# Optimization experiments

Hardware: AMD Instinct MI355X
Metric: run time of the kernel (lower is better)

Reference implementation:

```python
import jax, jax.numpy as jnp
import numpy as np

B = 4; IN_CH = 256; HEAD_CH = 64; NUM_CLS = 3; H = 128; W = 128
NH = 4; KEY = 16; VAL = 16; OUT_CH = 2
VX = 0.1 * 8; VY = 0.1 * 8  # voxel_size[:2] * out_size_factor
DW = 1.6; DL = 3.9; STRIDE = 1
C_CTR = (HEAD_CH + 2 + NUM_CLS) * 9      # 621
C_COR = (HEAD_CH + 2 + NUM_CLS * 4) * 8  # 624
C_FG = (HEAD_CH + 2 + NUM_CLS) * 9       # 621


def _sampler_points():
    offs = np.arange(-STRIDE, STRIDE + 1, STRIDE, dtype=np.float32)
    oy, ox = np.meshgrid(offs, offs, indexing='ij')
    ctr = np.stack([ox, oy], 0).reshape(2, 9)  # pixel offsets
    cx = np.array([-DW/2, -DW/2, DW/2, DW/2, DL/2, -DL/2, DL/2, -DL/2], np.float32) / VX
    cy = np.array([DL/2, -DL/2, DL/2, -DL/2, -DW/2, -DW/2, DW/2, DW/2], np.float32) / VY
    # faithful to torch: stack(dim=1) -> [8,2] then .view(2,8) (row-major reinterpret)
    cor = np.stack([cx, cy], 1).reshape(2, 8)
    r = max(DW, DL)
    fx = np.array([-r/3, -r/3, -r/3, 0, 0, 0, r/3, r/3, r/3], np.float32) / VX
    fy = np.array([-r/3, 0, r/3, -r/3, 0, r/3, -r/3, 0, r/3], np.float32) / VY
    fg = np.stack([fx, fy], 1).reshape(2, 9)
    return jnp.asarray(ctr), jnp.asarray(cor), jnp.asarray(fg)


def _raw_grid():
    gx = jnp.arange(W, dtype=jnp.float32) + 0.5
    gy = jnp.arange(H, dtype=jnp.float32) + 0.5
    return jnp.stack([jnp.broadcast_to(gx[None, :], (H, W)),
                      jnp.broadcast_to(gy[:, None], (H, W))], 0)  # [2,H,W]


def _conv3x3(x, w, b):
    y = jax.lax.conv_general_dilated(x, w, (1, 1), 'SAME',
                                     dimension_numbers=('NCHW', 'OIHW', 'NCHW'))
    return y + b[None, :, None, None]


def _cbr3(x, w, b, s, t):  # conv3x3 + inference-mode BN (folded scale/shift) + relu
    return jax.nn.relu(_conv3x3(x, w, b) * s[None, :, None, None] + t[None, :, None, None])


def _cbr1(x, w, b, s, t):  # per-head 1x1 conv + BN + relu, w: [NH,O,C], x: [B,C,H,W]
    y = jnp.einsum('noc,bchw->nbohw', w, x) + b[:, None, :, None, None]
    return jax.nn.relu(y * s[:, None, :, None, None] + t[:, None, :, None, None])


def _sample(feats, grids):
    # feats [B,C,H,W]; grids [2,n,H,W] pixel coords. Matches F.grid_sample
    # (bilinear, zeros padding, align_corners=False): sample at pixel coord g-0.5.
    n = grids.shape[1]
    geo = jnp.stack([grids[0] / W, grids[1] / H], 0)  # recover_coords, [2,n,H,W]
    gx, gy = grids[0] - 0.5, grids[1] - 0.5
    x0f = jnp.floor(gx); y0f = jnp.floor(gy)
    dx, dy = gx - x0f, gy - y0f
    x0 = x0f.astype(jnp.int32); y0 = y0f.astype(jnp.int32)
    flat = feats.reshape(B, -1, H * W)

    def gather(xc, yc, wgt):
        valid = ((xc >= 0) & (xc < W) & (yc >= 0) & (yc < H)).astype(feats.dtype) * wgt
        idx = jnp.clip(yc, 0, H - 1) * W + jnp.clip(xc, 0, W - 1)
        v = jnp.take(flat, idx.reshape(-1), axis=2).reshape(B, -1, n, H, W)
        return v * valid[None, None]

    s = (gather(x0, y0, (1 - dx) * (1 - dy)) + gather(x0 + 1, y0, dx * (1 - dy))
         + gather(x0, y0 + 1, (1 - dx) * dy) + gather(x0 + 1, y0 + 1, dx * dy))
    geo_b = jnp.broadcast_to(geo[None], (B,) + geo.shape)
    out = jnp.concatenate([s, geo_b], axis=1)  # [B,C+2,n,H,W]
    return out.reshape(B, -1, H, W)           # channel index = c*n + p, as torch .view


def _forward(base_feats, cc_w, cc_b, cc_s, cc_t, ch_w, ch_b,
             oc_w, oc_b, oc_s, oc_t, oh_w, oh_b,
             fc_w, fc_b, fc_s, fc_t, fh_w, fh_b,
             q_w, q_b, q_s, q_t,
             ck_w, ck_b, ck_s, ck_t, cv_w, cv_b, cv_s, cv_t,
             kk_w, kk_b, kk_s, kk_t, kv_w, kv_b, kv_s, kv_t,
             fk_w, fk_b, fk_s, fk_t, fv_w, fv_b, fv_s, fv_t,
             p1_w, p1_b, p1_s, p1_t, p2_w, p2_b):
    center_feat = _cbr3(base_feats, cc_w, cc_b, cc_s, cc_t)
    center_map = _conv3x3(center_feat, ch_w, ch_b)
    corner_feat = _cbr3(base_feats, oc_w, oc_b, oc_s, oc_t)
    corner_map = _conv3x3(corner_feat, oh_w, oh_b)
    fg_feat = _cbr3(base_feats, fc_w, fc_b, fc_s, fc_t)
    fg_map = _conv3x3(fg_feat, fh_w, fh_b)

    ctr_pts, cor_pts, fg_pts = _sampler_points()
    raw = _raw_grid()
    g_ctr = raw[:, None] + ctr_pts[:, :, None, None]  # [2,9,H,W]
    g_cor = raw[:, None] + cor_pts[:, :, None, None]  # [2,8,H,W]
    g_fg = raw[:, None] + fg_pts[:, :, None, None]    # [2,9,H,W]

    cs = _sample(jnp.concatenate([center_feat, center_map], 1), g_ctr)  # [B,621,H,W]
    os_ = _sample(jnp.concatenate([corner_feat, corner_map], 1), g_cor)  # [B,624,H,W]
    fs = _sample(jnp.concatenate([fg_feat, fg_map], 1), g_fg)            # [B,621,H,W]

    q = _cbr1(base_feats, q_w, q_b, q_s, q_t)  # [NH,B,KEY,H,W]
    ck = _cbr1(cs, ck_w, ck_b, ck_s, ck_t); cv = _cbr1(cs, cv_w, cv_b, cv_s, cv_t)
    ok = _cbr1(os_, kk_w, kk_b, kk_s, kk_t); ov = _cbr1(os_, kv_w, kv_b, kv_s, kv_t)
    fk = _cbr1(fs, fk_w, fk_b, fk_s, fk_t); fv = _cbr1(fs, fv_w, fv_b, fv_s, fv_t)

    logits = jnp.stack([(q * ck).sum(2), (q * ok).sum(2), (q * fk).sum(2)], axis=2)  # [NH,B,3,H,W]
    attw = jax.nn.softmax(logits, axis=2)
    vals = jnp.stack([cv, ov, fv], axis=2)          # [NH,B,3,VAL,H,W]
    att = (attw[:, :, :, None] * vals).sum(2)       # [NH,B,VAL,H,W]

    # predict: 1x1 conv over cat([base_feats, att]) + BN + relu, then 1x1 to out_ch
    h1 = (jnp.einsum('noc,bchw->nbohw', p1_w[:, :, :IN_CH], base_feats)
          + jnp.einsum('nov,nbvhw->nbohw', p1_w[:, :, IN_CH:], att)
          + p1_b[:, None, :, None, None])
    h1 = jax.nn.relu(h1 * p1_s[:, None, :, None, None] + p1_t[:, None, :, None, None])
    pred = jnp.einsum('npo,nbohw->nbphw', p2_w, h1) + p2_b[:, None, :, None, None]
    heads = jnp.moveaxis(pred, 0, 1).reshape(B, NH * OUT_CH, H, W)
    return jnp.concatenate([center_map, corner_map, fg_map, heads], axis=1)  # [B,26,H,W]


def setup_inputs() -> dict:
    ks = iter(jax.random.split(jax.random.key(0), 80))

    def rn(shape, s=0.05):
        return jax.random.normal(next(ks), shape, jnp.float32) * s

    d = {"base_feats": jax.random.normal(next(ks), (B, IN_CH, H, W), jnp.float32)}
    for conv, head, hc in (("cc", "ch", NUM_CLS), ("oc", "oh", NUM_CLS * 4), ("fc", "fh", NUM_CLS)):
        d[conv + "_w"] = rn((HEAD_CH, IN_CH, 3, 3)); d[conv + "_b"] = rn((HEAD_CH,))
        d[conv + "_s"] = 1.0 + rn((HEAD_CH,)); d[conv + "_t"] = rn((HEAD_CH,))
        d[head + "_w"] = rn((hc, HEAD_CH, 3, 3)); d[head + "_b"] = jnp.full((hc,), -2.19, jnp.float32)
    d["q_w"] = rn((NH, KEY, IN_CH)); d["q_b"] = rn((NH, KEY))
    d["q_s"] = 1.0 + rn((NH, KEY)); d["q_t"] = rn((NH, KEY))
    for name, cin, cout in (("ck", C_CTR, KEY), ("cv", C_CTR, VAL), ("kk", C_COR, KEY),
                            ("kv", C_COR, VAL), ("fk", C_FG, KEY), ("fv", C_FG, VAL)):
        d[name + "_w"] = rn((NH, cout, cin)); d[name + "_b"] = rn((NH, cout))
        d[name + "_s"] = 1.0 + rn((NH, cout)); d[name + "_t"] = rn((NH, cout))
    d["p1_w"] = rn((NH, HEAD_CH, IN_CH + VAL)); d["p1_b"] = rn((NH, HEAD_CH))
    d["p1_s"] = 1.0 + rn((NH, HEAD_CH)); d["p1_t"] = rn((NH, HEAD_CH))
    d["p2_w"] = rn((NH, OUT_CH, HEAD_CH)); d["p2_b"] = jnp.full((NH, OUT_CH), -2.19, jnp.float32)
    return d


def reference(base_feats, cc_w, cc_b, cc_s, cc_t, ch_w, ch_b,
              oc_w, oc_b, oc_s, oc_t, oh_w, oh_b,
              fc_w, fc_b, fc_s, fc_t, fh_w, fh_b,
              q_w, q_b, q_s, q_t,
              ck_w, ck_b, ck_s, ck_t, cv_w, cv_b, cv_s, cv_t,
              kk_w, kk_b, kk_s, kk_t, kv_w, kv_b, kv_s, kv_t,
              fk_w, fk_b, fk_s, fk_t, fv_w, fv_b, fv_s, fv_t,
              p1_w, p1_b, p1_s, p1_t, p2_w, p2_b):
    return _forward(base_feats, cc_w, cc_b, cc_s, cc_t, ch_w, ch_b,
                    oc_w, oc_b, oc_s, oc_t, oh_w, oh_b,
                    fc_w, fc_b, fc_s, fc_t, fh_w, fh_b,
                    q_w, q_b, q_s, q_t,
                    ck_w, ck_b, ck_s, ck_t, cv_w, cv_b, cv_s, cv_t,
                    kk_w, kk_b, kk_s, kk_t, kv_w, kv_b, kv_s, kv_t,
                    fk_w, fk_b, fk_s, fk_t, fv_w, fv_b, fv_s, fv_t,
                    p1_w, p1_b, p1_s, p1_t, p2_w, p2_b)
```

## Files before the change

### kernel.cpp

```cpp
#include <hip/hip_runtime.h>
#include <hip/hip_bf16.h>
#include <math.h>


#define HW 16384
#define WIMG 128

typedef unsigned short ushortT;
typedef __attribute__((ext_vector_type(8))) short short8;
typedef __attribute__((ext_vector_type(4))) float floatx4;
typedef __attribute__((ext_vector_type(4))) unsigned uintx4;

constexpr size_t OFF_KV    = 16777216;
constexpr size_t OFF_A16   = 29360128;
constexpr size_t OFF_B16   = 38012928;
constexpr size_t OFF_CWT   = 46057216;
constexpr size_t OFF_CB    = OFF_CWT + 221184;
constexpr size_t OFF_HWT   = OFF_CB + 192;
constexpr size_t OFF_QWT   = OFF_HWT + 13824;
constexpr size_t OFF_QB    = OFF_QWT + 8192;
constexpr size_t OFF_KVW   = OFF_QB + 64;
constexpr size_t OFF_GEO   = OFF_KVW + 266240;
constexpr size_t OFF_P1WT  = OFF_GEO + 1152;
constexpr size_t OFF_P1B   = OFF_P1WT + 40960;

struct P53 { const float* p[53]; };

__device__ inline ushortT f2bf(float f) {
    unsigned u = __float_as_uint(f);
    unsigned r = (u + 0x7FFFu + ((u >> 16) & 1u)) >> 16;
    return (ushortT)r;
}
__device__ inline unsigned packbf(float a, float b) {
    return (unsigned)f2bf(a) | ((unsigned)f2bf(b) << 16);
}
__device__ inline float bf2f(ushortT u) {
    return __uint_as_float((unsigned)u << 16);
}

typedef __attribute__((address_space(3))) ushortT lds_us;
typedef __attribute__((address_space(1))) const ushortT glb_us;
__device__ inline void gload_lds16(const ushortT* g, ushortT* ldsbase) {
    __builtin_amdgcn_global_load_lds((glb_us*)g, (lds_us*)ldsbase, 16, 0, 0);
}

__device__ const float c_ox[3][9] = {
    {-1.f, 0.f, 1.f, -1.f, 0.f, 1.f, -1.f, 0.f, 1.f},
    {-1.f, 2.4375f, -1.f, -2.4375f, 1.f, 2.4375f, 1.f, -2.4375f, 0.f},
    {-1.625f, -1.625f, -1.625f, 0.f, -1.625f, 1.625f, 0.f, -1.625f, 0.f}};
__device__ const float c_oy[3][9] = {
    {-1.f, -1.f, -1.f, 0.f, 0.f, 0.f, 1.f, 1.f, 1.f},
    {2.4375f, -1.f, -2.4375f, -1.f, 2.4375f, 1.f, -2.4375f, 1.f, 0.f},
    {0.f, 0.f, 1.625f, 1.625f, -1.625f, 1.625f, 0.f, 1.625f, 1.625f}};

__device__ const int tapX_cor[16] = {-1,-1, 2, 3,-1,-1,-3,-2, 1, 1, 2, 3, 1, 1,-3,-2};
__device__ const int tapY_cor[16] = { 2, 3,-1,-1,-3,-2,-1,-1, 2, 3, 1, 1,-3,-2, 1, 1};
__device__ const int tapR_cor[16] = { 4, 5, 2, 2, 0, 1, 2, 2, 4, 5, 3, 3, 0, 1, 3, 3};

__device__ inline float cornw(float off, int X) {
    float f = floorf(off);
    float d = off - f;
    int fi = (int)f;
    return (X == fi) ? (1.f - d) : (X == fi + 1) ? d : 0.f;
}

__global__ __launch_bounds__(256) void setup_kernel(P53 ptrs, float* __restrict__ ws,
                                                    const float* __restrict__ base,
                                                    ushortT* __restrict__ a16,
                                                    ushortT* __restrict__ b16) {
    int i = blockIdx.x * 256 + threadIdx.x;
    const float* const* p = ptrs.p;
    if (i < 1102464) {
        if (i < 442368) {
            int tap = i / 49152, r = i % 49152;
            int g = r / 1536, r2 = r % 1536;
            int M = r2 >> 3, j = r2 & 7;
            int br = M >> 6, oc = M & 63, ic = g * 8 + j;
            float v = p[1 + 6 * br][(oc * 256 + ic) * 9 + tap] * p[3 + 6 * br][oc];
            ((ushortT*)(ws + OFF_CWT))[i] = f2bf(v);
            return;
        }
        i -= 442368;
        if (i < 192) {
            int br = i >> 6, oc = i & 63;
            ws[OFF_CB + i] = p[2 + 6 * br][oc] * p[3 + 6 * br][oc] + p[4 + 6 * br][oc];
            return;
        }
        i -= 192;
        if (i < 27648) {
            int j = i & 7, m = (i >> 3) & 15, u = (i >> 7) % 72, br = i / 9216;
            int cnt = (br == 1) ? 12 : 3;
            int t = u >> 3, g = u & 7, ic = g * 8 + j;
            const float* hw = (br == 0) ? p[5] : (br == 1) ? p[11] : p[17];
            float v = (m < cnt) ? hw[(m * 64 + ic) * 9 + t] : 0.f;
            ((ushortT*)(ws + OFF_HWT))[i] = f2bf(v);
            return;
        }
        i -= 27648;
        if (i < 16384) {
            int j = i & 7, m = (i >> 3) & 63, sg = i >> 9;
            int k = (sg >> 2) * 32 + (sg & 3) * 8 + j;
            ((ushortT*)(ws + OFF_QWT))[i] = f2bf(p[19][m * 256 + k] * p[21][m]);
            return;
        }
        i -= 16384;
        if (i < 64) { ws[OFF_QB + i] = p[20][i] * p[21][i] + p[22][i]; return; }
        i -= 64;
        if (i < 532480) {
            int br, NQ, NTAP, n, C, i2;
            if (i < 110592)      { br = 0; NQ = 3; NTAP = 9;  n = 9; C = 67; i2 = i; }
            else if (i < 274432) { br = 1; NQ = 4; NTAP = 16; n = 8; C = 76; i2 = i - 110592; }
            else                 { br = 2; NQ = 7; NTAP = 25; n = 9; C = 67; i2 = i - 274432; }
            int gsz = NQ * 4096;
            int g = i2 / gsz, r = i2 % gsz;
            int q = r >> 12, r2 = r & 4095;
            int sub = r2 >> 10, m = (r2 >> 3) & 127, j = r2 & 7;
            int t = q * 4 + sub, c = g * 8 + j;
            float v = 0.f;
            if (t < NTAP && c < C) {
                int X, Y;
                if (br == 0)      { X = t % 3 - 1; Y = t / 3 - 1; }
                else if (br == 1) { X = tapX_cor[t]; Y = tapY_cor[t]; }
                else              { X = t % 5 - 2; Y = t / 5 - 2; }
                const float* wsrc = (m < 64) ? p[23 + 8 * br] : p[27 + 8 * br];
                int mo = (m < 64) ? m : m - 64;
                float sc = (m < 64) ? p[25 + 8 * br][mo] : p[29 + 8 * br][mo];
                int Cn = (C + 2) * n;
                float s = 0.f;
                for (int pp = 0; pp < n; ++pp) {
                    float ww = cornw(c_ox[br][pp], X) * cornw(c_oy[br][pp], Y);
                    if (ww != 0.f) s += ww * wsrc[mo * Cn + c * n + pp];
                }
                v = s * sc;
            }
            ((ushortT*)(ws + OFF_KVW))[i] = f2bf(v);
            return;
        }
        i -= 532480;
        if (i < 1152) {
            int br = i / 384, rem = i % 384, which = rem >> 7, m = rem & 127;
            int n = (br == 1) ? 8 : 9, C = (br == 1) ? 76 : 67, Cn = (C + 2) * n;
            const float* wsrc = (m < 64) ? p[23 + 8 * br] : p[27 + 8 * br];
            int mo = (m < 64) ? m : m - 64;
            float sc = (m < 64) ? p[25 + 8 * br][mo] : p[29 + 8 * br][mo];
            float bb = (m < 64) ? p[24 + 8 * br][mo] : p[28 + 8 * br][mo];
            float tt = (m < 64) ? p[26 + 8 * br][mo] : p[30 + 8 * br][mo];
            float v = 0.f;
            if (which == 0) {
                for (int pp = 0; pp < n; ++pp) v += wsrc[mo * Cn + C * n + pp];
                v *= sc;
            } else if (which == 1) {
                for (int pp = 0; pp < n; ++pp) v += wsrc[mo * Cn + (C + 1) * n + pp];
                v *= sc;
            } else {
                for (int pp = 0; pp < n; ++pp)
                    v += wsrc[mo * Cn + C * n + pp] * c_ox[br][pp]
                       + wsrc[mo * Cn + (C + 1) * n + pp] * c_oy[br][pp];
                v = v * sc * 0.0078125f + bb * sc + tt;
            }
            ws[OFF_GEO + br * 384 + which * 128 + m] = v;
            return;
        }
        i -= 1152;
        if (i < 81920) {
            int j = i & 7, M = (i >> 3) & 255, sg = i >> 11;
            int k = (sg >> 2) * 32 + (sg & 3) * 8 + j;
            int nh = M >> 6, oc = M & 63;
            float sc = p[49][nh * 64 + oc];
            float v;
            if (k < 256) v = p[47][(nh * 64 + oc) * 272 + k] * sc;
            else {
                int k2 = k - 256, nh2 = k2 >> 4, va = k2 & 15;
                v = (nh2 == nh) ? p[47][(nh * 64 + oc) * 272 + 256 + va] * sc : 0.f;
            }
            ((ushortT*)(ws + OFF_P1WT))[i] = f2bf(v);
            return;
        }
        i -= 81920;
        if (i < 256) { ws[OFF_P1B + i] = p[48][i] * p[49][i] + p[50][i]; }
        return;
    }
    int idx = i - 1102464;
    if (idx < 4 * 32 * 130 * 130) {
        int col = idx % 130, t = idx / 130;
        int row = t % 130; t /= 130;
        int icg = t & 31, b = t >> 5;
        int h = row - 1, w = col - 1;
        unsigned wds[4] = {0u, 0u, 0u, 0u};
        if ((unsigned)h < 128u && (unsigned)w < 128u) {
            const float* s = base + (size_t)(b * 256 + icg * 8) * HW + h * WIMG + w;
            #pragma unroll
            for (int jp = 0; jp < 4; ++jp)
                wds[jp] = packbf(s[(size_t)(2 * jp) * HW], s[(size_t)(2 * jp + 1) * HW]);
        }
        unsigned* d = (unsigned*)(a16 + (size_t)idx * 8);
        d[0] = wds[0]; d[1] = wds[1]; d[2] = wds[2]; d[3] = wds[3];
        return;
    }
    idx -= 4 * 32 * 130 * 130;
    if (idx < 4 * 28 * 134 * 134) {
        int col = idx % 134, row = (idx / 134) % 134;
        if (row < 3 || row >= 131 || col < 3 || col >= 131) {
            unsigned* d = (unsigned*)(b16 + (size_t)idx * 8);
            d[0] = 0u; d[1] = 0u; d[2] = 0u; d[3] = 0u;
        }
    }
}

__global__ __launch_bounds__(256) void conv_base_mfma(
    const ushortT* __restrict__ a16, const ushortT* __restrict__ wA,
    const float* __restrict__ cb, ushortT* __restrict__ b16)
{
    const int wv = threadIdx.x >> 6, lane = threadIdx.x & 63;
    const int sub = lane >> 4, ln = lane & 15;
    const int xh = blockIdx.x, h = blockIdx.y, b = blockIdx.z;
    const int x0 = xh * 64;
    __shared__ __align__(16) ushortT sbuf[2][792 * 8];

    floatx4 acc[3][4];
    #pragma unroll
    for (int mt = 0; mt < 3; ++mt)
        #pragma unroll
        for (int nt = 0; nt < 4; ++nt)
            #pragma unroll
            for (int r = 0; r < 4; ++r) acc[mt][nt][r] = 0.f;

    const int wbase = threadIdx.x & ~63;
    auto stage = [&](int s, int buf) {
        #pragma unroll
        for (int it = 0; it < 4; ++it) {
            int idx = threadIdx.x + it * 256;
            if (idx < 792) {
                int col = idx % 66, t2 = idx / 66;
                int r = t2 % 3, icg = t2 / 3;
                const ushortT* g = a16 +
                    (((size_t)(b * 32 + s * 4 + icg) * 130 + (h + r)) * 130 + (x0 + col)) * 8;
                gload_lds16(g, &sbuf[buf][(size_t)(it * 256 + wbase) * 8]);
            }
        }
    };
    stage(0, 0);
    for (int s = 0; s < 8; ++s) {
        __syncthreads();
        if (s < 7) stage(s + 1, (s + 1) & 1);
        const ushortT* sb = sbuf[s & 1];
        #pragma unroll
        for (int tap = 0; tap < 9; ++tap) {
            const int ky = tap / 3, kx = tap % 3;
            short8 Bf[4];
            #pragma unroll
            for (int nt = 0; nt < 4; ++nt) {
                int c = nt * 16 + ln + kx;
                Bf[nt] = *(const short8*)(sb + ((sub * 3 + ky) * 66 + c) * 8);
            }
            const int g = s * 4 + sub;
            short8 Af[3];
            #pragma unroll
            for (int mt = 0; mt < 3; ++mt) {
                int m = wv * 48 + mt * 16 + ln;
                Af[mt] = *(const short8*)(wA + (((size_t)tap * 32 + g) * 192 + m) * 8);
            }
            #pragma unroll
            for (int mt = 0; mt < 3; ++mt)
                #pragma unroll
                for (int nt = 0; nt < 4; ++nt)
                    acc[mt][nt] = __builtin_amdgcn_mfma_f32_16x16x32_bf16(
                        Af[mt], Bf[nt], acc[mt][nt], 0, 0, 0);
        }
    }
    #pragma unroll
    for (int mt = 0; mt < 3; ++mt) {
        int ocq = wv * 48 + mt * 16 + sub * 4;
        #pragma unroll
        for (int nt = 0; nt < 4; ++nt) {
            int px = x0 + nt * 16 + ln;
            float v0 = fmaxf(acc[mt][nt][0] + cb[ocq + 0], 0.f);
            float v1 = fmaxf(acc[mt][nt][1] + cb[ocq + 1], 0.f);
            float v2 = fmaxf(acc[mt][nt][2] + cb[ocq + 2], 0.f);
            float v3 = fmaxf(acc[mt][nt][3] + cb[ocq + 3], 0.f);
            unsigned lo = packbf(v0, v1), hi = packbf(v2, v3);
            unsigned plo = (unsigned)__shfl_down((int)lo, 16);
            unsigned phi = (unsigned)__shfl_down((int)hi, 16);
            if (!(sub & 1)) {
                int br = ocq >> 6, oc = ocq & 63;
                int grp = ((br == 0) ? 0 : (br == 1) ? 9 : 19) + (oc >> 3);
                uintx4 w = {lo, hi, plo, phi};
                *(uintx4*)(b16 +
                    (((size_t)(b * 28 + grp) * 134 + (h + 3)) * 134 + (px + 3)) * 8) = w;
            }
        }
    }
}

__global__ __launch_bounds__(256) void conv_head_mfma(
    const ushortT* __restrict__ b16c, const ushortT* __restrict__ wH,
    const float* __restrict__ chb, const float* __restrict__ ohb,
    const float* __restrict__ fhb, float* __restrict__ out,
    ushortT* __restrict__ b16)
{
    const int wv = threadIdx.x >> 6, lane = threadIdx.x & 63;
    const int sub = lane >> 4, ln = lane & 15;
    const int x0 = (blockIdx.x & 1) * 64, h = blockIdx.x >> 1;
    const int br = blockIdx.y % 3, b = blockIdx.y / 3;
    const int cnt = (br == 1) ? 12 : 3;
    const int mapb = (br == 0) ? 0 : (br == 1) ? 3 : 15;
    const int grpb = (br == 0) ? 0 : (br == 1) ? 9 : 19;
    const float* bias = (br == 0) ? chb : (br == 1) ? ohb : fhb;
    __shared__ __align__(16) ushortT sbuf[8 * 3 * 66 * 8];
    const int wbase = threadIdx.x & ~63;

    for (int it = 0; it < 7; ++it) {
        int idx = threadIdx.x + it * 256;
        if (idx < 1584) {
            int col = idx % 66, t2 = idx / 66;
            int r = t2 % 3, g = t2 / 3;
            const ushortT* gp = b16c +
                (((size_t)(b * 28 + grpb + g) * 134 + (h + r + 2)) * 134 + (x0 + col + 2)) * 8;
            gload_lds16(gp, sbuf + (size_t)(it * 256 + wbase) * 8);
        }
    }
    __syncthreads();

    floatx4 acc;
    #pragma unroll
    for (int r = 0; r < 4; ++r) acc[r] = 0.f;
    #pragma unroll
    for (int k = 0; k < 18; ++k) {
        int u = k * 4 + sub;
        int t = u >> 3, g = u & 7;
        int dxv = t % 3 - 1, ry = t / 3;
        short8 Af = *(const short8*)(wH + ((size_t)(br * 72 + u) * 16 + ln) * 8);
        int c = wv * 16 + ln + dxv + 1;
        short8 Bf = *(const short8*)(sbuf + ((g * 3 + ry) * 66 + c) * 8);
        acc = __builtin_amdgcn_mfma_f32_16x16x32_bf16(Af, Bf, acc, 0, 0, 0);
    }
    {
        int px = x0 + wv * 16 + ln;
        #pragma unroll
        for (int r = 0; r < 4; ++r) {
            int m = sub * 4 + r;
            if (m < cnt) {
                float v = acc[r] + bias[m];
                out[((size_t)b * 26 + mapb + m) * HW + h * WIMG + px] = v;
                int grp = grpb + 8 + (m >> 3), j = m & 7;
                b16[(((size_t)(b * 28 + grp) * 134 + (h + 3)) * 134 + (px + 3)) * 8 + j]
                    = f2bf(v);
            }
        }
    }
}

template<int BRV>
__device__ __forceinline__ void kv_body(
    const ushortT* __restrict__ b16, const ushortT* __restrict__ kvw,
    const float* __restrict__ geob, ushortT* __restrict__ kvout,
    ushortT* __restrict__ sbufRaw)
{
    constexpr int NG    = (BRV == 0) ? 9  : (BRV == 1) ? 10 : 9;
    constexpr int NTAP  = (BRV == 0) ? 9  : (BRV == 1) ? 16 : 25;
    constexpr int NQ    = (BRV == 0) ? 3  : (BRV == 1) ? 4  : 7;
    constexpr int ROWS  = (BRV == 0) ? 3  : (BRV == 1) ? 6  : 5;
    constexpr int COLS  = (BRV == 0) ? 66 : (BRV == 1) ? 70 : 68;
    constexpr int XMIN  = (BRV == 0) ? -1 : (BRV == 1) ? -3 : -2;
    constexpr int UBASE = (BRV == 0) ? 0  : (BRV == 1) ? 9  : 19;
    constexpr int NEL   = ROWS * COLS;
    constexpr int NIT   = (NEL + 255) / 256;
    constexpr int WBASE = (BRV == 0) ? 0 : (BRV == 1) ? 110592 : 274432;

    const int lane = threadIdx.x & 63, wv = threadIdx.x >> 6;
    const int sub = lane >> 4, ln = lane & 15;
    const int mw = wv >> 1, nw = wv & 1;
    const int x0 = blockIdx.x * 64, h = blockIdx.y;
    const int b = blockIdx.z & 3;

    const int wbase = threadIdx.x & ~63;
    const int thrB = (nw * 32 + ln) * 16;

    int boff[NQ];
    #pragma unroll
    for (int q = 0; q < NQ; ++q) {
        int t = q * 4 + sub;
        int dxv, ry;
        if (t >= NTAP)          { dxv = -XMIN; ry = 0; }
        else if (BRV == 0)      { dxv = t % 3 - 1; ry = t / 3; }
        else if (BRV == 1)      { dxv = tapX_cor[t]; ry = tapR_cor[t]; }
        else                    { dxv = t % 5 - 2; ry = t / 5; }
        boff[q] = (ry * COLS + (dxv - XMIN)) * 16 + thrB;
    }

    auto stage = [&](int g, int buf) {
        #pragma unroll
        for (int it = 0; it < NIT; ++it) {
            int idx = threadIdx.x + it * 256;
            if (idx < NEL) {
                int rw = idx / COLS, col = idx % COLS;
                int dy = (BRV == 1) ? ((rw < 3) ? rw - 3 : rw - 2) : (rw - ROWS / 2);
                const ushortT* gp = b16 +
                    (((size_t)(b * 28 + UBASE + g) * 134 + (h + dy + 3)) * 134
                     + (x0 + col + XMIN + 3)) * 8;
                gload_lds16(gp, sbufRaw + (size_t)buf * (NEL * 8)
                                        + (size_t)(it * 256 + wbase) * 8);
            }
        }
    };

    floatx4 acc[4][2];
    #pragma unroll
    for (int mt = 0; mt < 4; ++mt)
        #pragma unroll
        for (int nt = 0; nt < 2; ++nt)
            #pragma unroll
            for (int r = 0; r < 4; ++r) acc[mt][nt][r] = 0.f;

    const ushortT* wp0 = kvw + WBASE + (size_t)sub * 1024 + (mw * 64 + ln) * 8;

    stage(0, 0);
    __syncthreads();
    int cur = 0;
    for (int g = 0; g < NG; ++g) {
        const char* sb8 = (const char*)(sbufRaw + (size_t)cur * (NEL * 8));
        const ushortT* wg = wp0 + (size_t)g * (NQ * 4096);
        short8 A0[4], B0[2], A1[4], B1[2];
        auto ldf = [&](int q, short8 A[4], short8 B[2]) {
            const ushortT* wp = wg + (size_t)q * 4096;
            #pragma unroll
            for (int mt = 0; mt < 4; ++mt)
                A[mt] = *(const short8*)(wp + mt * 128);
            int bb = boff[q];
            #pragma unroll
            for (int nt = 0; nt < 2; ++nt)
                B[nt] = *(const short8*)(sb8 + bb + nt * 256);
        };
        auto dom = [&](short8 A[4], short8 B[2]) {
            #pragma unroll
            for (int mt = 0; mt < 4; ++mt)
                #pragma unroll
                for (int nt = 0; nt < 2; ++nt)
                    acc[mt][nt] = __builtin_amdgcn_mfma_f32_16x16x32_bf16(
                        A[mt], B[nt], acc[mt][nt], 0, 0, 0);
        };
        ldf(0, A0, B0);
        if (g + 1 < NG) stage(g + 1, cur ^ 1);
        #pragma unroll
        for (int q = 0; q < NQ; q += 2) {
            bool h1 = (q + 1 < NQ);
            if (h1) ldf(q + 1, A1, B1);
            dom(A0, B0);
            if (q + 2 < NQ) ldf(q + 2, A0, B0);
            if (h1) dom(A1, B1);
        }
        __syncthreads();
        cur ^= 1;
    }

    const float* geo = geob + BRV * 384;
    const float fy = (h + 0.5f) * 0.0078125f;
    #pragma unroll
    for (int mt = 0; mt < 4; ++mt)
        #pragma unroll
        for (int nt = 0; nt < 2; ++nt) {
            int px = x0 + nw * 32 + nt * 16 + ln;
            float fx = (px + 0.5f) * 0.0078125f;
            #pragma unroll
            for (int r = 0; r < 4; ++r) {
                int Mi = mw * 64 + mt * 16 + sub * 4 + r;
                float v = acc[mt][nt][r] + geo[Mi] * fx + geo[128 + Mi] * fy + geo[256 + Mi];
                kvout[((size_t)(BRV * 4 + b) * 128 + Mi) * HW + h * WIMG + px] =
                    f2bf(fmaxf(v, 0.f));
            }
        }
}

__global__ __launch_bounds__(256, 6) void kv_all2(
    const ushortT* __restrict__ b16, const ushortT* __restrict__ kvw,
    const float* __restrict__ geob, ushortT* __restrict__ kvout)
{
    __shared__ __align__(16) ushortT sbuf[2 * 420 * 8];
    const int brv = blockIdx.z >> 2;
    if (brv == 0)      kv_body<0>(b16, kvw, geob, kvout, sbuf);
    else if (brv == 1) kv_body<1>(b16, kvw, geob, kvout, sbuf);
    else               kv_body<2>(b16, kvw, geob, kvout, sbuf);
}

__global__ __launch_bounds__(256) void attn_pred_mfma(
    float* __restrict__ ws, const float* __restrict__ p2w,
    const float* __restrict__ p2b, float* __restrict__ out)
{
    const int wv = threadIdx.x >> 6, lane = threadIdx.x & 63;
    const int sub = lane >> 4, ln = lane & 15;
    const int px0 = blockIdx.x * 64, b = blockIdx.y;
    const ushortT* wP1 = (const ushortT*)(ws + OFF_P1WT);
    const ushortT* wQ  = (const ushortT*)(ws + OFF_QWT);
    const ushortT* a16 = (const ushortT*)(ws + OFF_A16);
    const ushortT* kv = (const ushortT*)(ws + OFF_KV);
    const float* p1b = ws + OFF_P1B;
    const float* qb  = ws + OFF_QB;
    __shared__ __align__(16) ushortT xbuf[40 * 64 * 8];
    __shared__ __align__(16) ushortT qld[64 * 64];

    const int mypx = threadIdx.x & 63, nh = threadIdx.x >> 6;
    const int gpx = px0 + mypx, hh = gpx >> 7, ww = gpx & 127;
    #pragma unroll
    for (int g2 = 0; g2 < 8; ++g2) {
        int g = nh * 8 + g2;
        const ushortT* gp = a16 +
            (((size_t)(b * 32 + g) * 130 + (hh + 1)) * 130 + (ww + 1)) * 8;
        gload_lds16(gp, xbuf + (size_t)g * 64 * 8);
    }
    __syncthreads();

    {
        floatx4 qacc[4];
        #pragma unroll
        for (int nt = 0; nt < 4; ++nt)
            #pragma unroll
            for (int r = 0; r < 4; ++r) qacc[nt][r] = 0.f;
        #pragma unroll
        for (int kk = 0; kk < 8; ++kk) {
            short8 Af = *(const short8*)(wQ + (((kk * 4 + sub) * 64) + wv * 16 + ln) * 8);
            #pragma unroll
            for (int nt = 0; nt < 4; ++nt) {
                short8 Bf = *(const short8*)(xbuf + (((kk * 4 + sub) * 64) + nt * 16 + ln) * 8);
                qacc[nt] = __builtin_amdgcn_mfma_f32_16x16x32_bf16(Af, Bf, qacc[nt], 0, 0, 0);
            }
        }
        #pragma unroll
        for (int nt = 0; nt < 4; ++nt)
            #pragma unroll
            for (int r = 0; r < 4; ++r) {
                int row = wv * 16 + sub * 4 + r;
                qld[row * 64 + nt * 16 + ln] = f2bf(fmaxf(qacc[nt][r] + qb[row], 0.f));
            }
    }
    __syncthreads();

    {
        float l[3];
        #pragma unroll
        for (int br = 0; br < 3; ++br) {
            float s = 0.f;
            #pragma unroll
            for (int ko = 0; ko < 16; ++ko)
                s = fmaf(bf2f(qld[(nh * 16 + ko) * 64 + mypx]),
                         bf2f(kv[(size_t)((br * 4 + b) * 128 + nh * 16 + ko) * HW + gpx]), s);
            l[br] = s;
        }
        float m = fmaxf(l[0], fmaxf(l[1], l[2]));
        float e0 = __expf(l[0] - m), e1 = __expf(l[1] - m), e2 = __expf(l[2] - m);
        float inv = 1.f / (e0 + e1 + e2);
        float aw0 = e0 * inv, aw1 = e1 * inv, aw2 = e2 * inv;
        #pragma unroll
        for (int vap = 0; vap < 8; ++vap) {
            int va0 = vap * 2, va1 = vap * 2 + 1;
            float a0 =
                aw0 * bf2f(kv[(size_t)((0 * 4 + b) * 128 + 64 + nh * 16 + va0) * HW + gpx]) +
                aw1 * bf2f(kv[(size_t)((1 * 4 + b) * 128 + 64 + nh * 16 + va0) * HW + gpx]) +
                aw2 * bf2f(kv[(size_t)((2 * 4 + b) * 128 + 64 + nh * 16 + va0) * HW + gpx]);
            float a1 =
                aw0 * bf2f(kv[(size_t)((0 * 4 + b) * 128 + 64 + nh * 16 + va1) * HW + gpx]) +
                aw1 * bf2f(kv[(size_t)((1 * 4 + b) * 128 + 64 + nh * 16 + va1) * HW + gpx]) +
                aw2 * bf2f(kv[(size_t)((2 * 4 + b) * 128 + 64 + nh * 16 + va1) * HW + gpx]);
            int g = 32 + nh * 2 + (vap >> 2), wo = vap & 3;
            ((unsigned*)xbuf)[(g * 64 + mypx) * 4 + wo] = packbf(a0, a1);
        }
    }
    __syncthreads();

    floatx4 acc[4][4];
    #pragma unroll
    for (int mt = 0; mt < 4; ++mt)
        #pragma unroll
        for (int nt = 0; nt < 4; ++nt)
            #pragma unroll
            for (int r = 0; r < 4; ++r) acc[mt][nt][r] = 0.f;
    #pragma unroll
    for (int kk = 0; kk < 10; ++kk) {
        short8 Bf[4];
        #pragma unroll
        for (int nt = 0; nt < 4; ++nt)
            Bf[nt] = *(const short8*)(xbuf + (((kk * 4 + sub) * 64) + nt * 16 + ln) * 8);
        #pragma unroll
        for (int mt = 0; mt < 4; ++mt) {
            short8 Af = *(const short8*)(wP1 +
                (((size_t)(kk * 4 + sub) * 256) + wv * 64 + mt * 16 + ln) * 8);
            #pragma unroll
            for (int nt = 0; nt < 4; ++nt)
                acc[mt][nt] = __builtin_amdgcn_mfma_f32_16x16x32_bf16(Af, Bf[nt], acc[mt][nt], 0, 0, 0);
        }
    }

    float po0[4] = {0.f, 0.f, 0.f, 0.f}, po1[4] = {0.f, 0.f, 0.f, 0.f};
    #pragma unroll
    for (int mt = 0; mt < 4; ++mt)
        #pragma unroll
        for (int r = 0; r < 4; ++r) {
            int oc = mt * 16 + sub * 4 + r;
            float bias = p1b[wv * 64 + oc];
            float w0 = p2w[(wv * 2 + 0) * 64 + oc];
            float w1 = p2w[(wv * 2 + 1) * 64 + oc];
            #pragma unroll
            for (int nt = 0; nt < 4; ++nt) {
                float hv = fmaxf(acc[mt][nt][r] + bias, 0.f);
                po0[nt] = fmaf(w0, hv, po0[nt]);
                po1[nt] = fmaf(w1, hv, po1[nt]);
            }
        }
    #pragma unroll
    for (int nt = 0; nt < 4; ++nt) {
        po0[nt] += __shfl_xor(po0[nt], 16);
        po0[nt] += __shfl_xor(po0[nt], 32);
        po1[nt] += __shfl_xor(po1[nt], 16);
        po1[nt] += __shfl_xor(po1[nt], 32);
    }
    if (sub == 0) {
        #pragma unroll
        for (int nt = 0; nt < 4; ++nt) {
            int px = px0 + nt * 16 + ln;
            out[((size_t)b * 26 + 18 + wv * 2 + 0) * HW + px] = po0[nt] + p2b[wv * 2 + 0];
            out[((size_t)b * 26 + 18 + wv * 2 + 1) * HW + px] = po1[nt] + p2b[wv * 2 + 1];
        }
    }
}

extern "C" void kernel_launch(void* const* d_in, const int* in_sizes, int n_in,
                              void* d_out, int out_size, void* d_ws, size_t ws_size,
                              hipStream_t stream) {
    (void)in_sizes; (void)n_in; (void)out_size; (void)ws_size;
    float* ws  = (float*)d_ws;
    float* out = (float*)d_out;
    const float* base = (const float*)d_in[0];
    P53 ptrs;
    for (int i = 0; i < 53; ++i) ptrs.p[i] = (const float*)d_in[i];

    ushortT* a16 = (ushortT*)(ws + OFF_A16);
    ushortT* b16 = (ushortT*)(ws + OFF_B16);
    ushortT* kvb = (ushortT*)(ws + OFF_KV);
    const ushortT* kvw = (const ushortT*)(ws + OFF_KVW);

    setup_kernel<<<20613, 256, 0, stream>>>(ptrs, ws, base, a16, b16);
    conv_base_mfma<<<dim3(2, 128, 4), 256, 0, stream>>>(
        a16, (const ushortT*)(ws + OFF_CWT), ws + OFF_CB, b16);
    conv_head_mfma<<<dim3(256, 12), 256, 0, stream>>>(
        b16, (const ushortT*)(ws + OFF_HWT),
        (const float*)d_in[6], (const float*)d_in[12], (const float*)d_in[18],
        out, b16);
    kv_all2<<<dim3(2, 128, 12), 256, 0, stream>>>(b16, kvw, ws + OFF_GEO, kvb);
    attn_pred_mfma<<<dim3(256, 4), 256, 0, stream>>>(ws, (const float*)d_in[51],
                                                     (const float*)d_in[52], out);
}
```

Baseline: 450.3 us.

## Remap conv blocks per XCD for row locality and defer LDS prefetch issue

Both conv_base_mfma and kv_all2 now use 1D grids whose block index is decoded so that each of the 8 XCDs gets a contiguous band of 16 image rows. Neighbouring rows that share halo input then hit the same XCD L2. The next-stage global-to-LDS prefetch is moved from the start of each stage to just before the last MFMA group, fenced with sched_barrier, so its issue no longer competes with the early fragment loads. kv_all2's launch bounds also rise from 6 to 8 waves per SIMD, which may force register spilling in exchange for higher occupancy.

```diff
diff --git a/kernel.cpp b/kernel.cpp
--- a/kernel.cpp
+++ b/kernel.cpp
@@ -213,8 +213,11 @@
 {
     const int wv = threadIdx.x >> 6, lane = threadIdx.x & 63;
     const int sub = lane >> 4, ln = lane & 15;
-    const int xh = blockIdx.x, h = blockIdx.y, b = blockIdx.z;
-    const int x0 = xh * 64;
+    const int bid = blockIdx.x;
+    const int xcd = bid & 7, j = bid >> 3;
+    const int h = xcd * 16 + (j & 15);
+    const int rem = j >> 4;
+    const int x0 = (rem & 1) * 64, b = rem >> 1;
     __shared__ __align__(16) ushortT sbuf[2][792 * 8];
 
     floatx4 acc[3][4];
@@ -242,7 +245,6 @@
     stage(0, 0);
     for (int s = 0; s < 8; ++s) {
         __syncthreads();
-        if (s < 7) stage(s + 1, (s + 1) & 1);
         const ushortT* sb = sbuf[s & 1];
         #pragma unroll
         for (int tap = 0; tap < 9; ++tap) {
@@ -259,6 +261,11 @@
             for (int mt = 0; mt < 3; ++mt) {
                 int m = wv * 48 + mt * 16 + ln;
                 Af[mt] = *(const short8*)(wA + (((size_t)tap * 32 + g) * 192 + m) * 8);
+            }
+            if (tap == 8 && s < 7) {
+                __builtin_amdgcn_sched_barrier(0);
+                stage(s + 1, (s + 1) & 1);
+                __builtin_amdgcn_sched_barrier(0);
             }
             #pragma unroll
             for (int mt = 0; mt < 3; ++mt)
@@ -354,7 +361,7 @@
 __device__ __forceinline__ void kv_body(
     const ushortT* __restrict__ b16, const ushortT* __restrict__ kvw,
     const float* __restrict__ geob, ushortT* __restrict__ kvout,
-    ushortT* __restrict__ sbufRaw)
+    ushortT* __restrict__ sbufRaw, int x0, int h, int b)
 {
     constexpr int NG    = (BRV == 0) ? 9  : (BRV == 1) ? 10 : 9;
     constexpr int NTAP  = (BRV == 0) ? 9  : (BRV == 1) ? 16 : 25;
@@ -370,8 +377,6 @@
     const int lane = threadIdx.x & 63, wv = threadIdx.x >> 6;
     const int sub = lane >> 4, ln = lane & 15;
     const int mw = wv >> 1, nw = wv & 1;
-    const int x0 = blockIdx.x * 64, h = blockIdx.y;
-    const int b = blockIdx.z & 3;
 
     const int wbase = threadIdx.x & ~63;
     const int thrB = (nw * 32 + ln) * 16;
@@ -440,13 +445,22 @@
                         A[mt], B[nt], acc[mt][nt], 0, 0, 0);
         };
         ldf(0, A0, B0);
-        if (g + 1 < NG) stage(g + 1, cur ^ 1);
         #pragma unroll
         for (int q = 0; q < NQ; q += 2) {
             bool h1 = (q + 1 < NQ);
             if (h1) ldf(q + 1, A1, B1);
+            if (!h1 && g + 1 < NG) {
+                __builtin_amdgcn_sched_barrier(0);
+                stage(g + 1, cur ^ 1);
+                __builtin_amdgcn_sched_barrier(0);
+            }
             dom(A0, B0);
             if (q + 2 < NQ) ldf(q + 2, A0, B0);
+            else if (h1 && g + 1 < NG) {
+                __builtin_amdgcn_sched_barrier(0);
+                stage(g + 1, cur ^ 1);
+                __builtin_amdgcn_sched_barrier(0);
+            }
             if (h1) dom(A1, B1);
         }
         __syncthreads();
@@ -471,15 +485,21 @@
         }
 }
 
-__global__ __launch_bounds__(256, 6) void kv_all2(
+__global__ __launch_bounds__(256, 8) void kv_all2(
     const ushortT* __restrict__ b16, const ushortT* __restrict__ kvw,
     const float* __restrict__ geob, ushortT* __restrict__ kvout)
 {
     __shared__ __align__(16) ushortT sbuf[2 * 420 * 8];
-    const int brv = blockIdx.z >> 2;
-    if (brv == 0)      kv_body<0>(b16, kvw, geob, kvout, sbuf);
-    else if (brv == 1) kv_body<1>(b16, kvw, geob, kvout, sbuf);
-    else               kv_body<2>(b16, kvw, geob, kvout, sbuf);
+    const int bid = blockIdx.x;
+    const int xcd = bid & 7, j = bid >> 3;
+    const int h = xcd * 16 + (j & 15);
+    const int rem = j >> 4;
+    const int x0 = (rem & 1) * 64;
+    const int z = rem >> 1;
+    const int brv = z >> 2, b = z & 3;
+    if (brv == 0)      kv_body<0>(b16, kvw, geob, kvout, sbuf, x0, h, b);
+    else if (brv == 1) kv_body<1>(b16, kvw, geob, kvout, sbuf, x0, h, b);
+    else               kv_body<2>(b16, kvw, geob, kvout, sbuf, x0, h, b);
 }
 
 __global__ __launch_bounds__(256) void attn_pred_mfma(
@@ -638,13 +658,13 @@
     const ushortT* kvw = (const ushortT*)(ws + OFF_KVW);
 
     setup_kernel<<<20613, 256, 0, stream>>>(ptrs, ws, base, a16, b16);
-    conv_base_mfma<<<dim3(2, 128, 4), 256, 0, stream>>>(
+    conv_base_mfma<<<1024, 256, 0, stream>>>(
         a16, (const ushortT*)(ws + OFF_CWT), ws + OFF_CB, b16);
     conv_head_mfma<<<dim3(256, 12), 256, 0, stream>>>(
         b16, (const ushortT*)(ws + OFF_HWT),
         (const float*)d_in[6], (const float*)d_in[12], (const float*)d_in[18],
         out, b16);
-    kv_all2<<<dim3(2, 128, 12), 256, 0, stream>>>(b16, kvw, ws + OFF_GEO, kvb);
+    kv_all2<<<3072, 256, 0, stream>>>(b16, kvw, ws + OFF_GEO, kvb);
     attn_pred_mfma<<<dim3(256, 4), 256, 0, stream>>>(ws, (const float*)d_in[51],
                                                      (const float*)d_in[52], out);
 }
```

New measurement: 461.4 us. +2.5%, slower.

## Halve kv conv pixel tile and stage all channel groups at once

Applied to the files above, without the earlier changes.

The kv convolution kernel now processes 32 pixels per block instead of 64, with each wave owning 32 output channels instead of a 64x32 tile, doubling the grid. Instead of double-buffering one channel group at a time with a barrier per group, it loads all groups (or two phases for the corner branch) into a larger shared buffer up front and then runs the MFMA loop with no intermediate syncs. This cuts barriers and raises block count and occupancy, at the cost of more halo reloads, more weight reads per output pixel, and no overlap between global loads and compute.

```diff
diff --git a/kernel.cpp b/kernel.cpp
--- a/kernel.cpp
+++ b/kernel.cpp
@@ -354,27 +354,26 @@
 __device__ __forceinline__ void kv_body(
     const ushortT* __restrict__ b16, const ushortT* __restrict__ kvw,
     const float* __restrict__ geob, ushortT* __restrict__ kvout,
-    ushortT* __restrict__ sbufRaw)
+    ushortT* __restrict__ sbuf)
 {
-    constexpr int NG    = (BRV == 0) ? 9  : (BRV == 1) ? 10 : 9;
-    constexpr int NTAP  = (BRV == 0) ? 9  : (BRV == 1) ? 16 : 25;
-    constexpr int NQ    = (BRV == 0) ? 3  : (BRV == 1) ? 4  : 7;
-    constexpr int ROWS  = (BRV == 0) ? 3  : (BRV == 1) ? 6  : 5;
-    constexpr int COLS  = (BRV == 0) ? 66 : (BRV == 1) ? 70 : 68;
-    constexpr int XMIN  = (BRV == 0) ? -1 : (BRV == 1) ? -3 : -2;
-    constexpr int UBASE = (BRV == 0) ? 0  : (BRV == 1) ? 9  : 19;
-    constexpr int NEL   = ROWS * COLS;
-    constexpr int NIT   = (NEL + 255) / 256;
+    constexpr int NGRP = (BRV == 0) ? 9 : (BRV == 1) ? 5 : 9;
+    constexpr int NPH  = (BRV == 1) ? 2 : 1;
+    constexpr int NTAP = (BRV == 0) ? 9 : (BRV == 1) ? 16 : 25;
+    constexpr int NQ   = (BRV == 0) ? 3 : (BRV == 1) ? 4 : 7;
+    constexpr int ROWS = (BRV == 0) ? 3 : (BRV == 1) ? 6 : 5;
+    constexpr int COLS = (BRV == 0) ? 34 : (BRV == 1) ? 38 : 36;
+    constexpr int XMIN = (BRV == 0) ? -1 : (BRV == 1) ? -3 : -2;
+    constexpr int UBASE = (BRV == 0) ? 0 : (BRV == 1) ? 9 : 19;
+    constexpr int NEL  = NGRP * ROWS * COLS;
+    constexpr int NIT  = (NEL + 255) / 256;
     constexpr int WBASE = (BRV == 0) ? 0 : (BRV == 1) ? 110592 : 274432;
 
     const int lane = threadIdx.x & 63, wv = threadIdx.x >> 6;
     const int sub = lane >> 4, ln = lane & 15;
-    const int mw = wv >> 1, nw = wv & 1;
-    const int x0 = blockIdx.x * 64, h = blockIdx.y;
+    const int x0 = blockIdx.x * 32, h = blockIdx.y;
     const int b = blockIdx.z & 3;
-
     const int wbase = threadIdx.x & ~63;
-    const int thrB = (nw * 32 + ln) * 16;
+    const int thrB = ln * 16;
 
     int boff[NQ];
     #pragma unroll
@@ -388,82 +387,79 @@
         boff[q] = (ry * COLS + (dxv - XMIN)) * 16 + thrB;
     }
 
-    auto stage = [&](int g, int buf) {
+    auto stage = [&](int ph) {
         #pragma unroll
         for (int it = 0; it < NIT; ++it) {
             int idx = threadIdx.x + it * 256;
             if (idx < NEL) {
-                int rw = idx / COLS, col = idx % COLS;
+                int grp = idx / (ROWS * COLS), r2 = idx % (ROWS * COLS);
+                int rw = r2 / COLS, col = r2 % COLS;
                 int dy = (BRV == 1) ? ((rw < 3) ? rw - 3 : rw - 2) : (rw - ROWS / 2);
                 const ushortT* gp = b16 +
-                    (((size_t)(b * 28 + UBASE + g) * 134 + (h + dy + 3)) * 134
+                    (((size_t)(b * 28 + UBASE + ph * NGRP + grp) * 134 + (h + dy + 3)) * 134
                      + (x0 + col + XMIN + 3)) * 8;
-                gload_lds16(gp, sbufRaw + (size_t)buf * (NEL * 8)
-                                        + (size_t)(it * 256 + wbase) * 8);
+                gload_lds16(gp, sbuf + (size_t)(it * 256 + wbase) * 8);
             }
         }
     };
 
-    floatx4 acc[4][2];
-    #pragma unroll
-    for (int mt = 0; mt < 4; ++mt)
+    floatx4 acc[2][2];
+    #pragma unroll
+    for (int mt = 0; mt < 2; ++mt)
         #pragma unroll
         for (int nt = 0; nt < 2; ++nt)
             #pragma unroll
             for (int r = 0; r < 4; ++r) acc[mt][nt][r] = 0.f;
 
-    const ushortT* wp0 = kvw + WBASE + (size_t)sub * 1024 + (mw * 64 + ln) * 8;
-
-    stage(0, 0);
-    __syncthreads();
-    int cur = 0;
-    for (int g = 0; g < NG; ++g) {
-        const char* sb8 = (const char*)(sbufRaw + (size_t)cur * (NEL * 8));
-        const ushortT* wg = wp0 + (size_t)g * (NQ * 4096);
-        short8 A0[4], B0[2], A1[4], B1[2];
-        auto ldf = [&](int q, short8 A[4], short8 B[2]) {
-            const ushortT* wp = wg + (size_t)q * 4096;
-            #pragma unroll
-            for (int mt = 0; mt < 4; ++mt)
-                A[mt] = *(const short8*)(wp + mt * 128);
-            int bb = boff[q];
-            #pragma unroll
-            for (int nt = 0; nt < 2; ++nt)
-                B[nt] = *(const short8*)(sb8 + bb + nt * 256);
-        };
-        auto dom = [&](short8 A[4], short8 B[2]) {
-            #pragma unroll
-            for (int mt = 0; mt < 4; ++mt)
+    for (int ph = 0; ph < NPH; ++ph) {
+        if (ph) __syncthreads();
+        stage(ph);
+        __syncthreads();
+        for (int g = 0; g < NGRP; ++g) {
+            const char* sb8 = (const char*)sbuf + g * (ROWS * COLS * 16);
+            const ushortT* wg = kvw + WBASE
+                + ((size_t)(ph * NGRP + g) * NQ) * 4096 + sub * 1024 + (wv * 32 + ln) * 8;
+            short8 A0[2], B0[2], A1[2], B1[2];
+            auto ldf = [&](int q, short8 A[2], short8 B[2]) {
+                #pragma unroll
+                for (int mt = 0; mt < 2; ++mt)
+                    A[mt] = *(const short8*)(wg + (size_t)q * 4096 + mt * 128);
+                int bb = boff[q];
                 #pragma unroll
                 for (int nt = 0; nt < 2; ++nt)
-                    acc[mt][nt] = __builtin_amdgcn_mfma_f32_16x16x32_bf16(
-                        A[mt], B[nt], acc[mt][nt], 0, 0, 0);
-        };
-        ldf(0, A0, B0);
-        if (g + 1 < NG) stage(g + 1, cur ^ 1);
-        #pragma unroll
-        for (int q = 0; q < NQ; q += 2) {
-            bool h1 = (q + 1 < NQ);
-            if (h1) ldf(q + 1, A1, B1);
-            dom(A0, B0);
-            if (q + 2 < NQ) ldf(q + 2, A0, B0);
-            if (h1) dom(A1, B1);
-        }
-        __syncthreads();
-        cur ^= 1;
+                    B[nt] = *(const short8*)(sb8 + bb + nt * 256);
+            };
+            auto dom = [&](short8 A[2], short8 B[2]) {
+                #pragma unroll
+                for (int mt = 0; mt < 2; ++mt)
+                    #pragma unroll
+                    for (int nt = 0; nt < 2; ++nt)
+                        acc[mt][nt] = __builtin_amdgcn_mfma_f32_16x16x32_bf16(
+                            A[mt], B[nt], acc[mt][nt], 0, 0, 0);
+            };
+            ldf(0, A0, B0);
+            #pragma unroll
+            for (int q = 0; q < NQ; q += 2) {
+                bool h1 = (q + 1 < NQ);
+                if (h1) ldf(q + 1, A1, B1);
+                dom(A0, B0);
+                if (q + 2 < NQ) ldf(q + 2, A0, B0);
+                if (h1) dom(A1, B1);
+            }
+        }
     }
 
     const float* geo = geob + BRV * 384;
     const float fy = (h + 0.5f) * 0.0078125f;
     #pragma unroll
-    for (int mt = 0; mt < 4; ++mt)
+    for (int mt = 0; mt < 2; ++mt)
         #pragma unroll
         for (int nt = 0; nt < 2; ++nt) {
-            int px = x0 + nw * 32 + nt * 16 + ln;
+            int px = x0 + nt * 16 + ln;
             float fx = (px + 0.5f) * 0.0078125f;
             #pragma unroll
             for (int r = 0; r < 4; ++r) {
-                int Mi = mw * 64 + mt * 16 + sub * 4 + r;
+                int Mi = wv * 32 + mt * 16 + sub * 4 + r;
                 float v = acc[mt][nt][r] + geo[Mi] * fx + geo[128 + Mi] * fy + geo[256 + Mi];
                 kvout[((size_t)(BRV * 4 + b) * 128 + Mi) * HW + h * WIMG + px] =
                     f2bf(fmaxf(v, 0.f));
@@ -471,11 +467,11 @@
         }
 }
 
-__global__ __launch_bounds__(256, 6) void kv_all2(
+__global__ __launch_bounds__(256, 6) void kv_all3(
     const ushortT* __restrict__ b16, const ushortT* __restrict__ kvw,
     const float* __restrict__ geob, ushortT* __restrict__ kvout)
 {
-    __shared__ __align__(16) ushortT sbuf[2 * 420 * 8];
+    __shared__ __align__(16) ushortT sbuf[1620 * 8];
     const int brv = blockIdx.z >> 2;
     if (brv == 0)      kv_body<0>(b16, kvw, geob, kvout, sbuf);
     else if (brv == 1) kv_body<1>(b16, kvw, geob, kvout, sbuf);
@@ -644,7 +640,7 @@
         b16, (const ushortT*)(ws + OFF_HWT),
         (const float*)d_in[6], (const float*)d_in[12], (const float*)d_in[18],
         out, b16);
-    kv_all2<<<dim3(2, 128, 12), 256, 0, stream>>>(b16, kvw, ws + OFF_GEO, kvb);
+    kv_all3<<<dim3(4, 128, 12), 256, 0, stream>>>(b16, kvw, ws + OFF_GEO, kvb);
     attn_pred_mfma<<<dim3(256, 4), 256, 0, stream>>>(ws, (const float*)d_in[51],
                                                      (const float*)d_in[52], out);
 }
```

After: 436.4 us. 1.03x faster.
